# Performance work log

Hardware: AMD Instinct MI355X
Metric: run time of the kernel (lower is better)

## Reference

```python
import jax, jax.numpy as jnp
import numpy as np

N = 100000      # nodes
E = 1600000     # edges (avg degree 16)
DIN = 128       # input_dim
H = 64          # hidden_dim -> intermediate width 2*H = 128
BN_EPS = 1e-5


def setup_inputs() -> dict:
    key = jax.random.key(0)
    ks = jax.random.split(key, 6)
    x = jax.random.normal(ks[0], (N, DIN), dtype=jnp.float32)
    edge_index = jax.random.randint(ks[1], (2, E), 0, N, dtype=jnp.int64)
    W1 = jax.random.normal(ks[2], (DIN, 2 * H), dtype=jnp.float32) / np.sqrt(DIN).astype(np.float32)
    b1 = jnp.zeros((2 * H,), jnp.float32)
    W2 = jax.random.normal(ks[3], (2 * H, H), dtype=jnp.float32) / np.sqrt(2 * H).astype(np.float32)
    b2 = jnp.zeros((H,), jnp.float32)
    gamma = jnp.ones((2 * H,), jnp.float32)
    beta = jnp.zeros((2 * H,), jnp.float32)
    prelu_a = jnp.asarray(0.25, jnp.float32)  # PReLU default single weight
    return {"x": x, "edge_index": edge_index, "W1": W1, "b1": b1,
            "W2": W2, "b2": b2, "gamma": gamma, "beta": beta, "prelu_a": prelu_a}


def _gcn_conv(x, W, b, src, dst, n):
    # PyG GCNConv (edge_weight=None): lin -> add self-loops -> sym-norm aggregate -> +bias
    h = x @ W                                             # [N, F]
    loops = jnp.arange(n, dtype=src.dtype)
    s = jnp.concatenate([src, loops])                     # [E+N]
    d = jnp.concatenate([dst, loops])
    deg = jax.ops.segment_sum(jnp.ones_like(s, jnp.float32), d, num_segments=n)
    dinv = jnp.where(deg > 0, jax.lax.rsqrt(deg), 0.0)    # deg^{-1/2}, 0 for isolated
    norm = dinv[s] * dinv[d]                              # [E+N]
    out = jax.ops.segment_sum(h[s] * norm[:, None], d, num_segments=n)
    return out + b


def reference(x, edge_index, W1, b1, W2, b2, gamma, beta, prelu_a):
    src, dst = edge_index[0], edge_index[1]
    z = _gcn_conv(x, W1, b1, src, dst, N)                 # conv1: [N, 2H]
    mean = jnp.mean(z, axis=0)                            # BatchNorm1d (training stats)
    var = jnp.var(z, axis=0)
    z = (z - mean) * (gamma * jax.lax.rsqrt(var + BN_EPS)) + beta
    z = jnp.where(z >= 0, z, prelu_a * z)                 # PReLU
    z = _gcn_conv(z, W2, b2, src, dst, N)                 # conv2: [N, H]
    return z
```

## Files before the change

kernel.cpp:

```cpp
#include <hip/hip_runtime.h>


#define DIN 128
#define F1  128
#define F2  64
#define BN_EPS 1e-5f
#define NODE_BSHIFT 8
#define NODE_BMASK  255
#define CHUNK 8192
#define PADB 4608

typedef __attribute__((ext_vector_type(8))) short bf16x8;
typedef __attribute__((ext_vector_type(8))) unsigned short u16x8;
typedef __attribute__((ext_vector_type(4))) float f32x4;
typedef __attribute__((ext_vector_type(2))) float f32x2;

__device__ __forceinline__ unsigned short f2bf(float f) {
    unsigned int u = __float_as_uint(f);
    u = u + 0x7fffu + ((u >> 16) & 1u);
    return (unsigned short)(u >> 16);
}
__device__ __forceinline__ float bf2f(unsigned short u) { return __uint_as_float((unsigned int)u << 16); }
__device__ __forceinline__ float bf_lo(unsigned int v) { return __uint_as_float(v << 16); }
__device__ __forceinline__ float bf_hi(unsigned int v) { return __uint_as_float(v & 0xffff0000u); }


__global__ __launch_bounds__(256) void wprep_k(const float* __restrict__ W1,
                                               const float* __restrict__ W2,
                                               unsigned short* __restrict__ wt1h,
                                               unsigned short* __restrict__ wt1l,
                                               unsigned short* __restrict__ wt2h,
                                               unsigned short* __restrict__ wt2l,
                                               int* __restrict__ bucketcur) {
    int t = blockIdx.x * 256 + threadIdx.x;
    if (t < 2048) {
        int c = t >> 4, k8 = (t & 15) * 8;
        u16x8 hv, lv;
#pragma unroll
        for (int j = 0; j < 8; j++) {
            float v = W1[(size_t)(k8 + j) * 128 + c];
            unsigned short hi = f2bf(v);
            hv[j] = hi;
            lv[j] = f2bf(v - bf2f(hi));
        }
        int addr = c * 128 + (((k8 >> 3) ^ (c & 15)) << 3);
        *(u16x8*)&wt1h[addr] = hv;
        *(u16x8*)&wt1l[addr] = lv;
    } else if (t < 3072) {
        int tt = t - 2048;
        int c = tt >> 4, k8 = (tt & 15) * 8;
        u16x8 hv, lv;
#pragma unroll
        for (int j = 0; j < 8; j++) {
            float v = W2[(size_t)(k8 + j) * 64 + c];
            unsigned short hi = f2bf(v);
            hv[j] = hi;
            lv[j] = f2bf(v - bf2f(hi));
        }
        int addr = c * 128 + (((k8 >> 3) ^ (c & 15)) << 3);
        *(u16x8*)&wt2h[addr] = hv;
        *(u16x8*)&wt2l[addr] = lv;
    } else if (t < 3584) {
        int b = t - 3072;
        bucketcur[b] = b * PADB;
    }
}


__global__ __launch_bounds__(256) void binpass_k(const int* __restrict__ src,
                                                 const int* __restrict__ dst,
                                                 int* __restrict__ bucketcur,
                                                 int2* __restrict__ pairs, int e) {
    __shared__ int lh[512], lbase[512], lrank[512];
    int t = threadIdx.x;
    for (int i = t; i < 512; i += 256) { lh[i] = 0; lrank[i] = 0; }
    __syncthreads();
    int base = blockIdx.x * CHUNK;
    int end = base + CHUNK; if (end > e) end = e;
    for (int i = base + t; i < end; i += 256)
        atomicAdd(&lh[dst[i] >> NODE_BSHIFT], 1);
    __syncthreads();
    for (int b = t; b < 512; b += 256) {
        int v = lh[b];
        lbase[b] = v ? atomicAdd(&bucketcur[b], v) : 0;
    }
    __syncthreads();
    for (int i = base + t; i < end; i += 256) {
        int sv = src[i], dv = dst[i];
        int b = dv >> NODE_BSHIFT;
        int r = atomicAdd(&lrank[b], 1);
        int idx = lbase[b] + r;
        if (idx < (b + 1) * PADB) pairs[idx] = make_int2(sv, dv);
    }
}


__global__ __launch_bounds__(256) void bucket_k(const int2* __restrict__ pairs,
                                                const int* __restrict__ bucketcur,
                                                float* __restrict__ dinv,
                                                int* __restrict__ rowptr,
                                                int* __restrict__ rowend,
                                                int* __restrict__ srcsorted, int n) {
    __shared__ int lh[256], loff[256], lrank[256];
    int b = blockIdx.x, t = threadIdx.x;
    int e0 = b * PADB;
    int e1 = bucketcur[b];
    lh[t] = 0;
    lrank[t] = 0;
    __syncthreads();
    for (int i = e0 + t; i < e1; i += 256)
        atomicAdd(&lh[pairs[i].y & NODE_BMASK], 1);
    __syncthreads();
    int deg = lh[t];
    int run = deg;
    for (int ofs = 1; ofs < 256; ofs <<= 1) {
        int y = (t >= ofs) ? lh[t - ofs] : 0;
        __syncthreads();
        run += y;
        lh[t] = run;
        __syncthreads();
    }
    loff[t] = run - deg;
    int node = (b << NODE_BSHIFT) + t;
    if (node < n) {
        dinv[node] = rsqrtf((float)(deg + 1));
        rowptr[node] = e0 + (run - deg);
        rowend[node] = e0 + run;
    }
    __syncthreads();
    for (int i = e0 + t; i < e1; i += 256) {
        int2 p = pairs[i];
        int lo = p.y & NODE_BMASK;
        int r = atomicAdd(&lrank[lo], 1);
        srcsorted[e0 + loff[lo] + r] = p.x;
    }
}


__global__ __launch_bounds__(512) void gemm1_k(const float* __restrict__ x,
                                               const unsigned short* __restrict__ wt1h,
                                               const unsigned short* __restrict__ wt1l,
                                               const float* __restrict__ dinv,
                                               unsigned int* __restrict__ h, int n) {
    __shared__ unsigned short wh[128 * 128];
    __shared__ unsigned short wl[128 * 128];
    int t = threadIdx.x;
    {
        const uint4* gh = (const uint4*)wt1h;
        const uint4* gl = (const uint4*)wt1l;
        uint4* dh = (uint4*)wh;
        uint4* dl = (uint4*)wl;
        for (int i = t; i < 2048; i += 512) { dh[i] = gh[i]; dl[i] = gl[i]; }
    }
    __syncthreads();

    int w = t >> 6, l = t & 63;
    int lr = l & 15, lg = l >> 4;
    int rowbase = blockIdx.x * 128;
    int arow = rowbase + w * 16 + lr;
    if (arow >= n) arow = n - 1;

    f32x4 acc[8];
#pragma unroll
    for (int nt = 0; nt < 8; nt++) acc[nt] = (f32x4)(0.0f);

#pragma unroll
    for (int ks = 0; ks < 4; ks++) {
        const float4* ap = (const float4*)(x + (size_t)arow * 128 + ks * 32 + lg * 8);
        float4 v0 = ap[0], v1 = ap[1];
        float vv[8] = {v0.x, v0.y, v0.z, v0.w, v1.x, v1.y, v1.z, v1.w};
        bf16x8 ah, al;
#pragma unroll
        for (int j = 0; j < 8; j++) {
            unsigned short hi = f2bf(vv[j]);
            ah[j] = (short)hi;
            al[j] = (short)f2bf(vv[j] - bf2f(hi));
        }
#pragma unroll
        for (int nt = 0; nt < 8; nt++) {
            int ao = (nt * 16 + lr) * 128 + (((4 * ks + lg) ^ lr) << 3);
            bf16x8 bh = *(const bf16x8*)&wh[ao];
            bf16x8 bl = *(const bf16x8*)&wl[ao];
            acc[nt] = __builtin_amdgcn_mfma_f32_16x16x32_bf16(ah, bh, acc[nt], 0, 0, 0);
            acc[nt] = __builtin_amdgcn_mfma_f32_16x16x32_bf16(al, bh, acc[nt], 0, 0, 0);
            acc[nt] = __builtin_amdgcn_mfma_f32_16x16x32_bf16(ah, bl, acc[nt], 0, 0, 0);
        }
    }
    __syncthreads();
    unsigned short* ob = wh;
#pragma unroll
    for (int r = 0; r < 4; r++) {
        int rl = w * 16 + lg * 4 + r;
        int grow = rowbase + rl;
        float di = dinv[grow < n ? grow : 0];
#pragma unroll
        for (int nt = 0; nt < 8; nt++)
            ob[rl * 128 + nt * 16 + lr] = f2bf(acc[nt][r] * di);
    }
    __syncthreads();
    const unsigned int* ob32 = (const unsigned int*)ob;
    for (int i = t; i < 128 * 64; i += 512) {
        int rl = i >> 6, cu = i & 63;
        int grow = rowbase + rl;
        if (grow < n) h[(size_t)grow * 64 + cu] = ob32[rl * 64 + cu];
    }
}


__global__ __launch_bounds__(64) void agg1_k(const unsigned int* __restrict__ h,
                                             const float* __restrict__ dinv,
                                             const int* __restrict__ rowptr,
                                             const int* __restrict__ rowend,
                                             const int* __restrict__ srcs,
                                             const float* __restrict__ b1,
                                             unsigned int* __restrict__ z, int n) {
    int nd = blockIdx.x;
    int f = threadIdx.x;
    float di = dinv[nd];
    unsigned int sv = h[(size_t)nd * 64 + f];
    float ax = bf_lo(sv);
    float ay = bf_hi(sv);
    int e = rowptr[nd], e1 = rowend[nd];
    for (; e + 16 <= e1; e += 16) {
        int s[16];
#pragma unroll
        for (int j = 0; j < 16; j++) s[j] = srcs[e + j];
        unsigned int v[16];
#pragma unroll
        for (int j = 0; j < 16; j++) v[j] = h[(size_t)s[j] * 64 + f];
#pragma unroll
        for (int j = 0; j < 16; j++) { ax += bf_lo(v[j]); ay += bf_hi(v[j]); }
    }
    for (; e + 8 <= e1; e += 8) {
        int s[8];
#pragma unroll
        for (int j = 0; j < 8; j++) s[j] = srcs[e + j];
        unsigned int v[8];
#pragma unroll
        for (int j = 0; j < 8; j++) v[j] = h[(size_t)s[j] * 64 + f];
#pragma unroll
        for (int j = 0; j < 8; j++) { ax += bf_lo(v[j]); ay += bf_hi(v[j]); }
    }
    for (; e + 4 <= e1; e += 4) {
        int s[4];
#pragma unroll
        for (int j = 0; j < 4; j++) s[j] = srcs[e + j];
        unsigned int v[4];
#pragma unroll
        for (int j = 0; j < 4; j++) v[j] = h[(size_t)s[j] * 64 + f];
#pragma unroll
        for (int j = 0; j < 4; j++) { ax += bf_lo(v[j]); ay += bf_hi(v[j]); }
    }
    for (; e < e1; e++) {
        unsigned int v = h[(size_t)srcs[e] * 64 + f];
        ax += bf_lo(v);
        ay += bf_hi(v);
    }
    float2 bb = ((const float2*)b1)[f];
    float ox = fmaf(ax, di, bb.x);
    float oy = fmaf(ay, di, bb.y);
    unsigned int zu = (unsigned int)f2bf(ox) | ((unsigned int)f2bf(oy) << 16);
    __builtin_nontemporal_store(zu, z + (size_t)nd * 64 + f);
}


__global__ __launch_bounds__(256) void bnstats_k(const unsigned int* __restrict__ zb,
                                                 double* __restrict__ bnacc, int n) {
    __shared__ float reds[8][128];
    __shared__ float redq[8][128];
    int t = threadIdx.x;
    int q = t >> 5;
    int c = t & 31;
    const uint2* z2 = (const uint2*)zb;
    float s0 = 0.f, s1 = 0.f, s2 = 0.f, s3 = 0.f;
    float q0 = 0.f, q1 = 0.f, q2 = 0.f, q3 = 0.f;
    int stride = gridDim.x * 8;
#pragma unroll 2
    for (int r = blockIdx.x * 8 + q; r < n; r += stride) {
        uint2 v = z2[(size_t)r * 32 + c];
        float a = bf_lo(v.x), b = bf_hi(v.x), cc = bf_lo(v.y), d = bf_hi(v.y);
        s0 += a; s1 += b; s2 += cc; s3 += d;
        q0 = fmaf(a, a, q0);
        q1 = fmaf(b, b, q1);
        q2 = fmaf(cc, cc, q2);
        q3 = fmaf(d, d, q3);
    }
    reds[q][c * 4]     = s0; redq[q][c * 4]     = q0;
    reds[q][c * 4 + 1] = s1; redq[q][c * 4 + 1] = q1;
    reds[q][c * 4 + 2] = s2; redq[q][c * 4 + 2] = q2;
    reds[q][c * 4 + 3] = s3; redq[q][c * 4 + 3] = q3;
    __syncthreads();
    if (t < 128) {
        float ssum = 0.f, qsum = 0.f;
#pragma unroll
        for (int i = 0; i < 8; i++) {
            ssum += reds[i][t];
            qsum += redq[i][t];
        }
        int copy = (blockIdx.x & 3) * 256;
        atomicAdd(&bnacc[copy + t], (double)ssum);
        atomicAdd(&bnacc[copy + 128 + t], (double)qsum);
    }
}


__global__ __launch_bounds__(512) void gemm2_k(const unsigned int* __restrict__ zb,
                                               const unsigned short* __restrict__ wt2h,
                                               const unsigned short* __restrict__ wt2l,
                                               const double* __restrict__ bnacc,
                                               const float* __restrict__ gamma,
                                               const float* __restrict__ beta,
                                               const float* __restrict__ prelu_a,
                                               const float* __restrict__ dinv,
                                               unsigned int* __restrict__ h2, int n) {
    __shared__ unsigned short wh[64 * 128];
    __shared__ unsigned short wl[64 * 128];
    __shared__ float lsc[128], lsh[128];
    int t = threadIdx.x;
    {
        const uint4* gh = (const uint4*)wt2h;
        const uint4* gl = (const uint4*)wt2l;
        uint4* dh = (uint4*)wh;
        uint4* dl = (uint4*)wl;
        for (int i = t; i < 1024; i += 512) { dh[i] = gh[i]; dl[i] = gl[i]; }
    }
    if (t < 128) {
        double sm = 0.0, qq = 0.0;
#pragma unroll
        for (int cpy = 0; cpy < 4; cpy++) {
            sm += bnacc[cpy * 256 + t];
            qq += bnacc[cpy * 256 + 128 + t];
        }
        double mean = sm / n;
        double var = qq / n - mean * mean;
        float sc = gamma[t] * rsqrtf((float)var + BN_EPS);
        lsc[t] = sc;
        lsh[t] = beta[t] - (float)mean * sc;
    }
    __syncthreads();

    float pa = prelu_a[0];
    int w = t >> 6, l = t & 63;
    int lr = l & 15, lg = l >> 4;
    int rowbase = blockIdx.x * 128;
    int arow = rowbase + w * 16 + lr;
    if (arow >= n) arow = n - 1;

    f32x4 acc[4];
#pragma unroll
    for (int nt = 0; nt < 4; nt++) acc[nt] = (f32x4)(0.0f);

#pragma unroll
    for (int ks = 0; ks < 4; ks++) {
        const uint4* ap = (const uint4*)(zb + (size_t)arow * 64 + ks * 16 + lg * 4);
        uint4 u = ap[0];
        const float4* sc4 = (const float4*)&lsc[ks * 32 + lg * 8];
        const float4* sh4 = (const float4*)&lsh[ks * 32 + lg * 8];
        float4 s0 = sc4[0], s1 = sc4[1];
        float4 t0 = sh4[0], t1 = sh4[1];
        float vv[8];
        vv[0] = fmaf(bf_lo(u.x), s0.x, t0.x); vv[1] = fmaf(bf_hi(u.x), s0.y, t0.y);
        vv[2] = fmaf(bf_lo(u.y), s0.z, t0.z); vv[3] = fmaf(bf_hi(u.y), s0.w, t0.w);
        vv[4] = fmaf(bf_lo(u.z), s1.x, t1.x); vv[5] = fmaf(bf_hi(u.z), s1.y, t1.y);
        vv[6] = fmaf(bf_lo(u.w), s1.z, t1.z); vv[7] = fmaf(bf_hi(u.w), s1.w, t1.w);
        bf16x8 ah, al;
#pragma unroll
        for (int j = 0; j < 8; j++) {
            float y = vv[j] >= 0.f ? vv[j] : pa * vv[j];
            unsigned short hi = f2bf(y);
            ah[j] = (short)hi;
            al[j] = (short)f2bf(y - bf2f(hi));
        }
#pragma unroll
        for (int nt = 0; nt < 4; nt++) {
            int ao = (nt * 16 + lr) * 128 + (((4 * ks + lg) ^ lr) << 3);
            bf16x8 bh = *(const bf16x8*)&wh[ao];
            bf16x8 bl = *(const bf16x8*)&wl[ao];
            acc[nt] = __builtin_amdgcn_mfma_f32_16x16x32_bf16(ah, bh, acc[nt], 0, 0, 0);
            acc[nt] = __builtin_amdgcn_mfma_f32_16x16x32_bf16(al, bh, acc[nt], 0, 0, 0);
            acc[nt] = __builtin_amdgcn_mfma_f32_16x16x32_bf16(ah, bl, acc[nt], 0, 0, 0);
        }
    }
    __syncthreads();
    unsigned short* ob = wh;
#pragma unroll
    for (int r = 0; r < 4; r++) {
        int rl = w * 16 + lg * 4 + r;
        int grow = rowbase + rl;
        float di = dinv[grow < n ? grow : 0];
#pragma unroll
        for (int nt = 0; nt < 4; nt++)
            ob[rl * 64 + nt * 16 + lr] = f2bf(acc[nt][r] * di);
    }
    __syncthreads();
    const unsigned int* ob32 = (const unsigned int*)ob;
    for (int i = t; i < 128 * 32; i += 512) {
        int rl = i >> 5, cu = i & 31;
        int grow = rowbase + rl;
        if (grow < n) h2[(size_t)grow * 32 + cu] = ob32[rl * 32 + cu];
    }
}


__global__ __launch_bounds__(64) void agg2_k(const unsigned short* __restrict__ hs,
                                             const float* __restrict__ dinv,
                                             const int* __restrict__ rowptr,
                                             const int* __restrict__ rowend,
                                             const int* __restrict__ srcs,
                                             const float* __restrict__ b2,
                                             float* __restrict__ out, int n) {
    int nd = blockIdx.x;
    int f = threadIdx.x;
    float di = dinv[nd];
    float acc = bf2f(hs[(size_t)nd * F2 + f]);
    int e = rowptr[nd], e1 = rowend[nd];
    for (; e + 16 <= e1; e += 16) {
        int s[16];
#pragma unroll
        for (int j = 0; j < 16; j++) s[j] = srcs[e + j];
        unsigned short v[16];
#pragma unroll
        for (int j = 0; j < 16; j++) v[j] = hs[(size_t)s[j] * F2 + f];
#pragma unroll
        for (int j = 0; j < 16; j++) acc += bf2f(v[j]);
    }
    for (; e + 8 <= e1; e += 8) {
        int s[8];
#pragma unroll
        for (int j = 0; j < 8; j++) s[j] = srcs[e + j];
        unsigned short v[8];
#pragma unroll
        for (int j = 0; j < 8; j++) v[j] = hs[(size_t)s[j] * F2 + f];
#pragma unroll
        for (int j = 0; j < 8; j++) acc += bf2f(v[j]);
    }
    for (; e + 4 <= e1; e += 4) {
        int s[4];
#pragma unroll
        for (int j = 0; j < 4; j++) s[j] = srcs[e + j];
        unsigned short v[4];
#pragma unroll
        for (int j = 0; j < 4; j++) v[j] = hs[(size_t)s[j] * F2 + f];
#pragma unroll
        for (int j = 0; j < 4; j++) acc += bf2f(v[j]);
    }
    for (; e < e1; e++)
        acc += bf2f(hs[(size_t)srcs[e] * F2 + f]);
    float o = fmaf(acc, di, b2[f]);
    __builtin_nontemporal_store(o, out + (size_t)nd * F2 + f);
}


extern "C" void kernel_launch(void* const* d_in, const int* in_sizes, int n_in,
                              void* d_out, int out_size, void* d_ws, size_t ws_size,
                              hipStream_t stream) {
    const float* x       = (const float*)d_in[0];
    const int*   ei      = (const int*)d_in[1];
    const float* W1      = (const float*)d_in[2];
    const float* b1      = (const float*)d_in[3];
    const float* W2      = (const float*)d_in[4];
    const float* b2      = (const float*)d_in[5];
    const float* gamma   = (const float*)d_in[6];
    const float* beta    = (const float*)d_in[7];
    const float* prelu_a = (const float*)d_in[8];

    const int N = in_sizes[0] / DIN;
    const int E = in_sizes[1] / 2;
    const int* src = ei;
    const int* dst = ei + E;
    const int NBUCK = (N + NODE_BMASK) >> NODE_BSHIFT;

    char* p = (char*)d_ws;
    size_t off = 0;
    auto take = [&](size_t bytes) -> char* {
        char* r = p + off;
        off = (off + bytes + 255) & ~(size_t)255;
        return r;
    };
    int*            bucketcur  = (int*)take(512 * 4);
    float*          dinv       = (float*)take((size_t)N * 4);
    int*            rowptr     = (int*)take((size_t)N * 4);
    int*            rowend     = (int*)take((size_t)N * 4);
    int*            srcsorted  = (int*)take((size_t)512 * PADB * 4);
    int2*           pairs      = (int2*)take((size_t)512 * PADB * 8);
    double*         bnacc      = (double*)take(4 * 256 * 8);
    unsigned short* wt1h       = (unsigned short*)take(128 * 128 * 2);
    unsigned short* wt1l       = (unsigned short*)take(128 * 128 * 2);
    unsigned short* wt2h       = (unsigned short*)take(64 * 128 * 2);
    unsigned short* wt2l       = (unsigned short*)take(64 * 128 * 2);
    unsigned int*   h          = (unsigned int*)take((size_t)N * 64 * 4);
    unsigned int*   z          = (unsigned int*)take((size_t)N * 64 * 4);
    unsigned int*   h2         = h;
    float*          out        = (float*)d_out;

    hipMemsetAsync(bnacc, 0, 4 * 256 * 8, stream);

    const int eb = (E + CHUNK - 1) / CHUNK;

    wprep_k<<<14, 256, 0, stream>>>(W1, W2, wt1h, wt1l, wt2h, wt2l, bucketcur);
    binpass_k<<<eb, 256, 0, stream>>>(src, dst, bucketcur, pairs, E);
    bucket_k<<<NBUCK, 256, 0, stream>>>(pairs, bucketcur, dinv, rowptr, rowend, srcsorted, N);

    gemm1_k<<<(N + 127) / 128, 512, 0, stream>>>(x, wt1h, wt1l, dinv, h, N);
    agg1_k<<<N, 64, 0, stream>>>(h, dinv, rowptr, rowend, srcsorted, b1, z, N);
    bnstats_k<<<1024, 256, 0, stream>>>(z, bnacc, N);
    gemm2_k<<<(N + 127) / 128, 512, 0, stream>>>(z, wt2h, wt2l, bnacc, gamma, beta, prelu_a, dinv, h2, N);
    agg2_k<<<N, F2, 0, stream>>>((const unsigned short*)h2, dinv, rowptr, rowend, srcsorted, b2, out, N);
}
```

Before: 304.0 us.

## Fold weight prep into binning kernel and pack four nodes per aggregation block

The weight-split prep kernel is merged into the edge-binning kernel as extra blocks, and the per-bucket cursor init is replaced by a zeroed counter folded into the existing memset. This removes one kernel launch and its serialization point. The two aggregation kernels now run four nodes per 256-thread block instead of one node per 64-thread block, which cuts the block count fourfold and reduces scheduling overhead. A node-range guard is added because of the new blocking.

```diff
diff --git a/kernel.cpp b/kernel.cpp
--- a/kernel.cpp
+++ b/kernel.cpp
@@ -25,52 +25,48 @@
 __device__ __forceinline__ float bf_hi(unsigned int v) { return __uint_as_float(v & 0xffff0000u); }
 
 
-__global__ __launch_bounds__(256) void wprep_k(const float* __restrict__ W1,
-                                               const float* __restrict__ W2,
-                                               unsigned short* __restrict__ wt1h,
-                                               unsigned short* __restrict__ wt1l,
-                                               unsigned short* __restrict__ wt2h,
-                                               unsigned short* __restrict__ wt2l,
-                                               int* __restrict__ bucketcur) {
-    int t = blockIdx.x * 256 + threadIdx.x;
-    if (t < 2048) {
-        int c = t >> 4, k8 = (t & 15) * 8;
-        u16x8 hv, lv;
-#pragma unroll
-        for (int j = 0; j < 8; j++) {
-            float v = W1[(size_t)(k8 + j) * 128 + c];
-            unsigned short hi = f2bf(v);
-            hv[j] = hi;
-            lv[j] = f2bf(v - bf2f(hi));
-        }
-        int addr = c * 128 + (((k8 >> 3) ^ (c & 15)) << 3);
-        *(u16x8*)&wt1h[addr] = hv;
-        *(u16x8*)&wt1l[addr] = lv;
-    } else if (t < 3072) {
-        int tt = t - 2048;
-        int c = tt >> 4, k8 = (tt & 15) * 8;
-        u16x8 hv, lv;
-#pragma unroll
-        for (int j = 0; j < 8; j++) {
-            float v = W2[(size_t)(k8 + j) * 64 + c];
-            unsigned short hi = f2bf(v);
-            hv[j] = hi;
-            lv[j] = f2bf(v - bf2f(hi));
-        }
-        int addr = c * 128 + (((k8 >> 3) ^ (c & 15)) << 3);
-        *(u16x8*)&wt2h[addr] = hv;
-        *(u16x8*)&wt2l[addr] = lv;
-    } else if (t < 3584) {
-        int b = t - 3072;
-        bucketcur[b] = b * PADB;
-    }
-}
-
-
 __global__ __launch_bounds__(256) void binpass_k(const int* __restrict__ src,
                                                  const int* __restrict__ dst,
-                                                 int* __restrict__ bucketcur,
-                                                 int2* __restrict__ pairs, int e) {
+                                                 int* __restrict__ bucketcnt,
+                                                 int2* __restrict__ pairs, int e, int eb,
+                                                 const float* __restrict__ W1,
+                                                 const float* __restrict__ W2,
+                                                 unsigned short* __restrict__ wt1h,
+                                                 unsigned short* __restrict__ wt1l,
+                                                 unsigned short* __restrict__ wt2h,
+                                                 unsigned short* __restrict__ wt2l) {
+    if (blockIdx.x >= eb) {
+        int t = (blockIdx.x - eb) * 256 + threadIdx.x;
+        if (t < 2048) {
+            int c = t >> 4, k8 = (t & 15) * 8;
+            u16x8 hv, lv;
+#pragma unroll
+            for (int j = 0; j < 8; j++) {
+                float v = W1[(size_t)(k8 + j) * 128 + c];
+                unsigned short hi = f2bf(v);
+                hv[j] = hi;
+                lv[j] = f2bf(v - bf2f(hi));
+            }
+            int addr = c * 128 + (((k8 >> 3) ^ (c & 15)) << 3);
+            *(u16x8*)&wt1h[addr] = hv;
+            *(u16x8*)&wt1l[addr] = lv;
+        } else if (t < 3072) {
+            int tt = t - 2048;
+            int c = tt >> 4, k8 = (tt & 15) * 8;
+            u16x8 hv, lv;
+#pragma unroll
+            for (int j = 0; j < 8; j++) {
+                float v = W2[(size_t)(k8 + j) * 64 + c];
+                unsigned short hi = f2bf(v);
+                hv[j] = hi;
+                lv[j] = f2bf(v - bf2f(hi));
+            }
+            int addr = c * 128 + (((k8 >> 3) ^ (c & 15)) << 3);
+            *(u16x8*)&wt2h[addr] = hv;
+            *(u16x8*)&wt2l[addr] = lv;
+        }
+        return;
+    }
     __shared__ int lh[512], lbase[512], lrank[512];
     int t = threadIdx.x;
     for (int i = t; i < 512; i += 256) { lh[i] = 0; lrank[i] = 0; }
@@ -82,7 +78,7 @@
     __syncthreads();
     for (int b = t; b < 512; b += 256) {
         int v = lh[b];
-        lbase[b] = v ? atomicAdd(&bucketcur[b], v) : 0;
+        lbase[b] = v ? (b * PADB + atomicAdd(&bucketcnt[b], v)) : 0;
     }
     __syncthreads();
     for (int i = base + t; i < end; i += 256) {
@@ -96,7 +92,7 @@
 
 
 __global__ __launch_bounds__(256) void bucket_k(const int2* __restrict__ pairs,
-                                                const int* __restrict__ bucketcur,
+                                                const int* __restrict__ bucketcnt,
                                                 float* __restrict__ dinv,
                                                 int* __restrict__ rowptr,
                                                 int* __restrict__ rowend,
@@ -104,7 +100,7 @@
     __shared__ int lh[256], loff[256], lrank[256];
     int b = blockIdx.x, t = threadIdx.x;
     int e0 = b * PADB;
-    int e1 = bucketcur[b];
+    int e1 = e0 + bucketcnt[b];
     lh[t] = 0;
     lrank[t] = 0;
     __syncthreads();
@@ -207,15 +203,16 @@
 }
 
 
-__global__ __launch_bounds__(64) void agg1_k(const unsigned int* __restrict__ h,
-                                             const float* __restrict__ dinv,
-                                             const int* __restrict__ rowptr,
-                                             const int* __restrict__ rowend,
-                                             const int* __restrict__ srcs,
-                                             const float* __restrict__ b1,
-                                             unsigned int* __restrict__ z, int n) {
-    int nd = blockIdx.x;
-    int f = threadIdx.x;
+__global__ __launch_bounds__(256) void agg1_k(const unsigned int* __restrict__ h,
+                                              const float* __restrict__ dinv,
+                                              const int* __restrict__ rowptr,
+                                              const int* __restrict__ rowend,
+                                              const int* __restrict__ srcs,
+                                              const float* __restrict__ b1,
+                                              unsigned int* __restrict__ z, int n) {
+    int nd = blockIdx.x * 4 + (threadIdx.x >> 6);
+    if (nd >= n) return;
+    int f = threadIdx.x & 63;
     float di = dinv[nd];
     unsigned int sv = h[(size_t)nd * 64 + f];
     float ax = bf_lo(sv);
@@ -402,15 +399,16 @@
 }
 
 
-__global__ __launch_bounds__(64) void agg2_k(const unsigned short* __restrict__ hs,
-                                             const float* __restrict__ dinv,
-                                             const int* __restrict__ rowptr,
-                                             const int* __restrict__ rowend,
-                                             const int* __restrict__ srcs,
-                                             const float* __restrict__ b2,
-                                             float* __restrict__ out, int n) {
-    int nd = blockIdx.x;
-    int f = threadIdx.x;
+__global__ __launch_bounds__(256) void agg2_k(const unsigned short* __restrict__ hs,
+                                              const float* __restrict__ dinv,
+                                              const int* __restrict__ rowptr,
+                                              const int* __restrict__ rowend,
+                                              const int* __restrict__ srcs,
+                                              const float* __restrict__ b2,
+                                              float* __restrict__ out, int n) {
+    int nd = blockIdx.x * 4 + (threadIdx.x >> 6);
+    if (nd >= n) return;
+    int f = threadIdx.x & 63;
     float di = dinv[nd];
     float acc = bf2f(hs[(size_t)nd * F2 + f]);
     int e = rowptr[nd], e1 = rowend[nd];
@@ -477,13 +475,13 @@
         off = (off + bytes + 255) & ~(size_t)255;
         return r;
     };
-    int*            bucketcur  = (int*)take(512 * 4);
+    int*            bucketcnt  = (int*)take(512 * 4);
+    double*         bnacc      = (double*)take(4 * 256 * 8);
     float*          dinv       = (float*)take((size_t)N * 4);
     int*            rowptr     = (int*)take((size_t)N * 4);
     int*            rowend     = (int*)take((size_t)N * 4);
     int*            srcsorted  = (int*)take((size_t)512 * PADB * 4);
     int2*           pairs      = (int2*)take((size_t)512 * PADB * 8);
-    double*         bnacc      = (double*)take(4 * 256 * 8);
     unsigned short* wt1h       = (unsigned short*)take(128 * 128 * 2);
     unsigned short* wt1l       = (unsigned short*)take(128 * 128 * 2);
     unsigned short* wt2h       = (unsigned short*)take(64 * 128 * 2);
@@ -493,17 +491,17 @@
     unsigned int*   h2         = h;
     float*          out        = (float*)d_out;
 
-    hipMemsetAsync(bnacc, 0, 4 * 256 * 8, stream);
+    hipMemsetAsync(bucketcnt, 0, 512 * 4 + 4 * 256 * 8, stream);
 
     const int eb = (E + CHUNK - 1) / CHUNK;
 
-    wprep_k<<<14, 256, 0, stream>>>(W1, W2, wt1h, wt1l, wt2h, wt2l, bucketcur);
-    binpass_k<<<eb, 256, 0, stream>>>(src, dst, bucketcur, pairs, E);
-    bucket_k<<<NBUCK, 256, 0, stream>>>(pairs, bucketcur, dinv, rowptr, rowend, srcsorted, N);
+    binpass_k<<<eb + 12, 256, 0, stream>>>(src, dst, bucketcnt, pairs, E, eb,
+                                           W1, W2, wt1h, wt1l, wt2h, wt2l);
+    bucket_k<<<NBUCK, 256, 0, stream>>>(pairs, bucketcnt, dinv, rowptr, rowend, srcsorted, N);
 
     gemm1_k<<<(N + 127) / 128, 512, 0, stream>>>(x, wt1h, wt1l, dinv, h, N);
-    agg1_k<<<N, 64, 0, stream>>>(h, dinv, rowptr, rowend, srcsorted, b1, z, N);
+    agg1_k<<<(N + 3) / 4, 256, 0, stream>>>(h, dinv, rowptr, rowend, srcsorted, b1, z, N);
     bnstats_k<<<1024, 256, 0, stream>>>(z, bnacc, N);
     gemm2_k<<<(N + 127) / 128, 512, 0, stream>>>(z, wt2h, wt2l, bnacc, gamma, beta, prelu_a, dinv, h2, N);
-    agg2_k<<<N, F2, 0, stream>>>((const unsigned short*)h2, dinv, rowptr, rowend, srcsorted, b2, out, N);
-}
+    agg2_k<<<(N + 3) / 4, 256, 0, stream>>>((const unsigned short*)h2, dinv, rowptr, rowend, srcsorted, b2, out, N);
+}
```

Measured after the change: 316.7 us. 4.2% more time.
